# Kernel tuning notes

Hardware: AMD Instinct MI355X
Metric: run time of the kernel (lower is better)

## Reference

```python
import jax, jax.numpy as jnp
import numpy as np

# pywt db4 decomposition filters
DEC_LO = jnp.array([-0.010597401784997278, 0.032883011666982945, 0.030841381835986965, -0.18703481171888114, -0.02798376941698385, 0.6308807679295904, 0.7148465705525415, 0.23037781330885523], dtype=jnp.float32)
DEC_HI = jnp.array([-0.23037781330885523, 0.7148465705525415, -0.6308807679295904, -0.02798376941698385, 0.18703481171888114, 0.030841381835986965, -0.032883011666982945, -0.010597401784997278], dtype=jnp.float32)

def _dwt_step(x):
    # single-level DWT along last axis, pywt 'symmetric' mode; x: [N, n]
    L = DEC_LO.shape[0]
    xe = jnp.pad(x, ((0, 0), (L - 1, L - 1)), mode='symmetric')[:, 1:]
    k = jnp.stack([DEC_LO[::-1], DEC_HI[::-1]])[:, None, :]  # [2,1,L]
    y = jax.lax.conv_general_dilated(xe[:, None, :], k, window_strides=(2,), padding='VALID')
    return y[:, 0, :], y[:, 1, :]  # cA, cD, each [N, (n+L-1)//2]

def _wavedec(x, level):
    a, dets = x, []
    for _ in range(level):
        a, d = _dwt_step(a)
        dets.append(d)
    return [a] + dets[::-1]  # [cA_L, cD_L, ..., cD_1]

def _wavelet_kan(x, basis, scales=5):
    # torch code detaches x before pywt.wavedec -> stop_gradient for faithful bwd
    coeffs = _wavedec(jax.lax.stop_gradient(x), scales - 1)
    out = 0.0
    for s in range(scales):
        c = coeffs[s]
        out = out + c @ basis[s][:c.shape[1], :]
    return out

def _dendritic(x, W, b):
    # W: [branches, in, out]; max over branches of GELU(Linear)
    h = jnp.einsum('ni,kio->kno', x, W) + b[:, None, :]
    return jnp.max(jax.nn.gelu(h, approximate=False), axis=0)

def _layernorm(x, g, b, eps=1e-5):
    m = jnp.mean(x, -1, keepdims=True)
    v = jnp.var(x, -1, keepdims=True)
    return (x - m) * jax.lax.rsqrt(v + eps) * g + b

def setup_inputs():
    key = jax.random.key(0)
    ks = jax.random.split(key, 12)
    N, D, H, M, Z, K, E = 16384, 768, 512, 256, 256, 20, 262144
    inp = {}
    inp['x'] = jax.random.normal(ks[0], (N, D), jnp.float32)
    inp['adj_rows'] = jax.random.randint(ks[1], (E,), 0, N, jnp.int32)
    inp['adj_cols'] = jax.random.randint(ks[2], (E,), 0, N, jnp.int32)
    inp['adj_vals'] = jax.random.uniform(ks[3], (E,), jnp.float32)
    inp['basis_enc'] = jax.random.normal(ks[4], (5, D, H), jnp.float32)
    inp['ln_g'] = jnp.ones((H,), jnp.float32)
    inp['ln_b'] = jnp.zeros((H,), jnp.float32)
    inp['Wd_enc'] = jax.random.normal(ks[5], (K, H, M), jnp.float32) * 0.04
    inp['bd_enc'] = jnp.zeros((K, M), jnp.float32)
    inp['W_mu'] = jax.random.normal(ks[6], (M, Z), jnp.float32) * 0.06
    inp['b_mu'] = jnp.zeros((Z,), jnp.float32)
    inp['W_lv'] = jax.random.normal(ks[7], (M, Z), jnp.float32) * 0.06
    inp['b_lv'] = jnp.zeros((Z,), jnp.float32)
    inp['Wd_dec'] = jax.random.normal(ks[8], (K, Z, H), jnp.float32) * 0.06
    inp['bd_dec'] = jnp.zeros((K, H), jnp.float32)
    inp['basis_dec'] = jax.random.normal(ks[9], (5, H, D), jnp.float32)
    inp['eps'] = jax.random.normal(ks[10], (N, Z), jnp.float32)
    return inp

def reference(x, adj_rows, adj_cols, adj_vals, basis_enc, ln_g, ln_b, Wd_enc, bd_enc, W_mu, b_mu, W_lv, b_lv, Wd_dec, bd_dec, basis_dec, eps):
    N = x.shape[0]
    # torch.sparse.mm(adj, x) with COO adj
    xa = jax.ops.segment_sum(adj_vals[:, None] * x[adj_cols], adj_rows, num_segments=N)
    h = _wavelet_kan(xa, basis_enc)
    h = _layernorm(h, ln_g, ln_b)
    enc = _dendritic(h, Wd_enc, bd_enc)
    mu = enc @ W_mu + b_mu
    logvar = enc @ W_lv + b_lv
    z = mu + eps * jnp.exp(0.5 * logvar)
    dec = _dendritic(z, Wd_dec, bd_dec)
    recon = _wavelet_kan(dec, basis_dec)
    return recon, mu, logvar
```

## Files before the change

kernel.cpp:

```cpp
#include <hip/hip_runtime.h>

typedef __attribute__((ext_vector_type(8))) short short8v;
typedef __attribute__((ext_vector_type(8))) unsigned short ushort8v;
typedef __attribute__((ext_vector_type(4))) float float4v;

__device__ __constant__ float c_LO[8] = {
    -0.010597401784997278f, 0.032883011666982945f, 0.030841381835986965f,
    -0.18703481171888114f, -0.02798376941698385f, 0.6308807679295904f,
    0.7148465705525415f, 0.23037781330885523f};
__device__ __constant__ float c_HI[8] = {
    -0.23037781330885523f, 0.7148465705525415f, -0.6308807679295904f,
    -0.02798376941698385f, 0.18703481171888114f, 0.030841381835986965f,
    -0.032883011666982945f, -0.010597401784997278f};

__device__ __forceinline__ unsigned short f2bf(float f) {
    unsigned u = __builtin_bit_cast(unsigned, f);
    unsigned r = u + 0x7fffu + ((u >> 16) & 1u);
    return (unsigned short)(r >> 16);
}
__device__ __forceinline__ float bf2f(unsigned short u) {
    return __builtin_bit_cast(float, (unsigned)u << 16);
}

__device__ __forceinline__ float gelu_fast(float x) {
    float x3 = x * x * x;
    float y = fmaf(0.044715f, x3, x) * 0.7978845608028654f;
    float t = fminf(fmaxf(y * 2.8853900817779268f, -30.f), 30.f);
    float e = exp2f(t);
    return x * e * __builtin_amdgcn_rcpf(e + 1.0f);
}

__device__ __forceinline__ void gload_lds16(const void* g, void* l) {
    __builtin_amdgcn_global_load_lds(g, l, 16, 0, 0);
}

__device__ __forceinline__ void dwt_lvl(const float* __restrict__ in, int n, float* __restrict__ outA,
                                        unsigned short* __restrict__ outD, int m, int lane) {
    for (int j = lane; j < m; j += 64) {
        float a = 0.f, d = 0.f;
#pragma unroll
        for (int i = 0; i < 8; ++i) {
            int p = 2 * j + 7 - i;
            int q = (p < 6) ? (5 - p) : ((p < n + 6) ? (p - 6) : (2 * n + 5 - p));
            float xv = in[q];
            a = fmaf(c_LO[i], xv, a);
            d = fmaf(c_HI[i], xv, d);
        }
        outA[j] = a;
        outD[j] = f2bf(d);
    }
}
__device__ __forceinline__ void dwt_lvl_final(const float* __restrict__ in, int n, unsigned short* __restrict__ outA,
                                              unsigned short* __restrict__ outD, int m, int lane) {
    for (int j = lane; j < m; j += 64) {
        float a = 0.f, d = 0.f;
#pragma unroll
        for (int i = 0; i < 8; ++i) {
            int p = 2 * j + 7 - i;
            int q = (p < 6) ? (5 - p) : ((p < n + 6) ? (p - 6) : (2 * n + 5 - p));
            float xv = in[q];
            a = fmaf(c_LO[i], xv, a);
            d = fmaf(c_HI[i], xv, d);
        }
        outA[j] = f2bf(a);
        outD[j] = f2bf(d);
    }
}

__global__ void cast_bf16_kernel(const float* __restrict__ in, unsigned short* __restrict__ out, int n4) {
    int i = blockIdx.x * blockDim.x + threadIdx.x;
    if (i >= n4) return;
    float4 v = ((const float4*)in)[i];
    ushort4 o;
    o.x = f2bf(v.x); o.y = f2bf(v.y); o.z = f2bf(v.z); o.w = f2bf(v.w);
    ((ushort4*)out)[i] = o;
}

__global__ void hist_kernel(const int* __restrict__ rows, int* __restrict__ cnt, int E) {
    int i = blockIdx.x * blockDim.x + threadIdx.x;
    if (i < E) atomicAdd(&cnt[rows[i]], 1);
}

__global__ __launch_bounds__(1024) void scan_kernel(const int* __restrict__ cnt, int* __restrict__ offs,
                                                    int* __restrict__ cursor, int Nrows, int E) {
    __shared__ int part[1024];
    int tid = threadIdx.x;
    const int per = Nrows / 1024;
    int base = tid * per;
    int local[16];
    int s = 0;
    for (int i = 0; i < per; ++i) { local[i] = s; s += cnt[base + i]; }
    part[tid] = s;
    __syncthreads();
    for (int off = 1; off < 1024; off <<= 1) {
        int v = part[tid];
        int w = (tid >= off) ? part[tid - off] : 0;
        __syncthreads();
        part[tid] = v + w;
        __syncthreads();
    }
    int pre = (tid == 0) ? 0 : part[tid - 1];
    for (int i = 0; i < per; ++i) {
        int o = pre + local[i];
        offs[base + i] = o;
        cursor[base + i] = o;
    }
    if (tid == 0) offs[Nrows] = E;
}

__global__ void scatter_kernel(const int* __restrict__ rows, const int* __restrict__ cols,
                               const float* __restrict__ vals, int* __restrict__ cursor,
                               int* __restrict__ ccol, float* __restrict__ cval, int E) {
    int i = blockIdx.x * blockDim.x + threadIdx.x;
    if (i >= E) return;
    int r = rows[i];
    int p = atomicAdd(&cursor[r], 1);
    ccol[p] = cols[i];
    cval[p] = vals[i];
}

__global__ __launch_bounds__(256) void spmm_wavedec_enc(const unsigned short* __restrict__ xb,
                                                        const int* __restrict__ offs,
                                                        const int* __restrict__ ccol,
                                                        const float* __restrict__ cval,
                                                        unsigned short* __restrict__ cenc) {
    __shared__ float buf0[4][768];
    __shared__ float buf1[4][400];
    const int widx = threadIdx.x >> 6, lane = threadIdx.x & 63;
    const int r = blockIdx.x * 4 + widx;
    float* b0 = buf0[widx];
    float* b1 = buf1[widx];

    int s = offs[r], e = offs[r + 1];
    float acc[12] = {};
    for (int j = s; j < e; ++j) {
        int c = ccol[j];
        float v = cval[j];
        const unsigned short* xr = xb + (size_t)c * 768;
#pragma unroll
        for (int seg = 0; seg < 3; ++seg) {
            ushort4 u = *(const ushort4*)(xr + seg * 256 + lane * 4);
            acc[seg * 4 + 0] = fmaf(v, bf2f(u.x), acc[seg * 4 + 0]);
            acc[seg * 4 + 1] = fmaf(v, bf2f(u.y), acc[seg * 4 + 1]);
            acc[seg * 4 + 2] = fmaf(v, bf2f(u.z), acc[seg * 4 + 2]);
            acc[seg * 4 + 3] = fmaf(v, bf2f(u.w), acc[seg * 4 + 3]);
        }
    }
#pragma unroll
    for (int seg = 0; seg < 3; ++seg) {
        b0[seg * 256 + lane * 4 + 0] = acc[seg * 4 + 0];
        b0[seg * 256 + lane * 4 + 1] = acc[seg * 4 + 1];
        b0[seg * 256 + lane * 4 + 2] = acc[seg * 4 + 2];
        b0[seg * 256 + lane * 4 + 3] = acc[seg * 4 + 3];
    }
    __syncthreads();

    unsigned short* cr = cenc + (size_t)r * 800;
    dwt_lvl(b0, 768, b1, cr + 407, 387, lane);
    __syncthreads();
    dwt_lvl(b1, 387, b0, cr + 210, 197, lane);
    __syncthreads();
    dwt_lvl(b0, 197, b1, cr + 108, 102, lane);
    __syncthreads();
    dwt_lvl_final(b1, 102, cr + 0, cr + 54, 54, lane);
    if (lane < 6) cr[794 + lane] = 0;
}

__global__ __launch_bounds__(256) void wavedec_dec(const unsigned short* __restrict__ decb,
                                                   unsigned short* __restrict__ cdec) {
    __shared__ float buf0[4][512];
    __shared__ float buf1[4][272];
    const int widx = threadIdx.x >> 6, lane = threadIdx.x & 63;
    const int r = blockIdx.x * 4 + widx;
    float* b0 = buf0[widx];
    float* b1 = buf1[widx];
    const unsigned short* ip = decb + (size_t)r * 512;
    for (int i = lane; i < 512; i += 64) b0[i] = bf2f(ip[i]);
    __syncthreads();
    unsigned short* cr = cdec + (size_t)r * 544;
    dwt_lvl(b0, 512, b1, cr + 279, 259, lane);
    __syncthreads();
    dwt_lvl(b1, 259, b0, cr + 146, 133, lane);
    __syncthreads();
    dwt_lvl(b0, 133, b1, cr + 76, 70, lane);
    __syncthreads();
    dwt_lvl_final(b1, 70, cr + 0, cr + 38, 38, lane);
    if (lane < 6) cr[538 + lane] = 0;
}

struct Bounds { int b[6]; };

__global__ void pack_basis_T(const float* __restrict__ basis, unsigned short* __restrict__ BT,
                             Bounds bd, int brows, int N, int K, int Kpad) {
    int idx = blockIdx.x * blockDim.x + threadIdx.x;
    if (idx >= N * Kpad) return;
    int n = idx / Kpad, k = idx - n * Kpad;
    float v = 0.f;
    if (k < K) {
        int s = 0;
#pragma unroll
        for (int t = 1; t < 5; ++t)
            if (k >= bd.b[t]) s = t;
        int lr = k - bd.b[s];
        v = basis[((size_t)s * brows + lr) * N + n];
    }
    BT[idx] = f2bf(v);
}

__global__ void pack_wT(const float* __restrict__ W, unsigned short* __restrict__ WT,
                        int NB, int K, int N, int Kpad) {
    int idx = blockIdx.x * blockDim.x + threadIdx.x;
    int tot = NB * N * Kpad;
    if (idx >= tot) return;
    int b = idx / (N * Kpad);
    int r = idx - b * (N * Kpad);
    int n = r / Kpad, k = r - n * Kpad;
    float v = (k < K) ? W[((size_t)b * K + k) * N + n] : 0.f;
    WT[idx] = f2bf(v);
}

template <int MODE>
__global__ __launch_bounds__(256) void gemm_mfma(const unsigned short* __restrict__ A,
                                                 const unsigned short* __restrict__ BT,
                                                 const float* __restrict__ bias,
                                                 const float* __restrict__ bias2,
                                                 void* __restrict__ Cv, void* __restrict__ Cv2,
                                                 int M, int N, int K, int lda, int ldb, int ldc, int nx) {
    __shared__ __align__(16) unsigned short As[128 * 32];
    __shared__ __align__(16) unsigned short Bs[128 * 32];
    const int tid = threadIdx.x;
    const int wave = tid >> 6, lane = tid & 63;
    const int nwg = gridDim.x;
    const int logical = (blockIdx.x & 7) * (nwg >> 3) + (blockIdx.x >> 3);
    const int mblk = logical / nx, nblk = logical - mblk * nx;
    const int m0 = mblk * 128, n0 = nblk * 128;
    const int wr = wave >> 1, wc = wave & 1;
    const int frow = lane & 15, fq = lane >> 4;

    const int off0 = tid * 16;
    const int r0 = off0 >> 6, c0 = off0 & 63;
    const int r1 = (off0 + 4096) >> 6, c1 = (off0 + 4096) & 63;
    const char* Ab = (const char*)A;
    const char* Bb = (const char*)BT;
    size_t gA0 = (size_t)(m0 + r0) * lda * 2 + c0;
    size_t gA1 = (size_t)(m0 + r1) * lda * 2 + c1;
    size_t gB0 = (size_t)(n0 + r0) * ldb * 2 + c0;
    size_t gB1 = (size_t)(n0 + r1) * ldb * 2 + c1;
    char* lA0 = (char*)As + wave * 1024;
    char* lB0 = (char*)Bs + wave * 1024;

    const int aoff = (wr * 64 + frow) * 32 + fq * 8;
    const int boff = (wc * 64 + frow) * 32 + fq * 8;

    float4v acc[4][4] = {};
    for (int k0 = 0; k0 < K; k0 += 32) {
        size_t kb2 = (size_t)k0 * 2;
        gload_lds16(Ab + gA0 + kb2, lA0);
        gload_lds16(Ab + gA1 + kb2, lA0 + 4096);
        gload_lds16(Bb + gB0 + kb2, lB0);
        gload_lds16(Bb + gB1 + kb2, lB0 + 4096);
        __syncthreads();
        short8v av[4], bv[4];
#pragma unroll
        for (int i = 0; i < 4; ++i) av[i] = *(const short8v*)(As + aoff + i * 512);
#pragma unroll
        for (int i = 0; i < 4; ++i) bv[i] = *(const short8v*)(Bs + boff + i * 512);
#pragma unroll
        for (int mi = 0; mi < 4; ++mi)
#pragma unroll
            for (int ni = 0; ni < 4; ++ni)
                acc[mi][ni] = __builtin_amdgcn_mfma_f32_16x16x32_bf16(av[mi], bv[ni], acc[mi][ni], 0, 0, 0);
        __syncthreads();
    }
#pragma unroll
    for (int ni = 0; ni < 4; ++ni) {
        int col = n0 + wc * 64 + ni * 16 + frow;
        float bval;
        float* dst;
        int coll;
        if (MODE == 2) {
            bool isMu = col < 256;
            coll = col & 255;
            bval = isMu ? bias[coll] : bias2[coll];
            dst = (float*)(isMu ? Cv : Cv2);
        } else {
            coll = col;
            bval = bias ? bias[col] : 0.f;
            dst = (float*)Cv;
        }
#pragma unroll
        for (int mi = 0; mi < 4; ++mi) {
#pragma unroll
            for (int i = 0; i < 4; ++i) {
                int row = m0 + wr * 64 + mi * 16 + fq * 4 + i;
                float v = acc[mi][ni][i] + bval;
                if (MODE == 2)
                    dst[(size_t)row * 256 + coll] = v;
                else
                    dst[(size_t)row * ldc + coll] = v;
            }
        }
    }
}

__global__ __launch_bounds__(256, 2) void dendritic_full(const unsigned short* __restrict__ A,
                                                         const unsigned short* __restrict__ WT,
                                                         const float* __restrict__ bias,
                                                         unsigned short* __restrict__ out,
                                                         int M, int Nc, int K, int nb, int nx) {
    __shared__ __align__(16) unsigned short As[128 * 64];
    __shared__ __align__(16) unsigned short Bs[2][64 * 64];
    const int tid = threadIdx.x;
    const int wave = tid >> 6;
    const int lane = tid & 63;

    const int nwg = gridDim.x;
    const int logical = (blockIdx.x & 7) * (nwg >> 3) + (blockIdx.x >> 3);
    const int mblk = logical / nx;
    const int nblk = logical - mblk * nx;
    const int n0 = nblk * 64, m0 = mblk * 128;

    const int wr = wave >> 1, wc = wave & 1;
    const int frow = lane & 15, fq = lane >> 4;

    int srA[4], scA[4];
#pragma unroll
    for (int i = 0; i < 4; ++i) {
        int ch = i * 256 + tid;
        srA[i] = ch >> 3;
        scA[i] = ((ch & 7) ^ (srA[i] & 7)) * 16;
    }
    int srB[2], scB[2];
#pragma unroll
    for (int i = 0; i < 2; ++i) {
        int ch = i * 256 + tid;
        srB[i] = ch >> 3;
        scB[i] = ((ch & 7) ^ (srB[i] & 7)) * 16;
    }
    const char* Ab = (const char*)A;
    const size_t K2 = (size_t)K * 2;
    const size_t branchBytes = (size_t)Nc * K2;
    char* lA  = (char*)As + wave * 1024;
    char* lB0 = (char*)&Bs[0][0] + wave * 1024;
    char* lB1 = (char*)&Bs[1][0] + wave * 1024;

    float4v hmn[4][2], hmx[4][2];
#pragma unroll
    for (int mi = 0; mi < 4; ++mi)
#pragma unroll
        for (int ni = 0; ni < 2; ++ni) { hmn[mi][ni] = (float4v)(1e30f); hmx[mi][ni] = (float4v)(-1e30f); }

    const int npair = nb >> 1;
    for (int p = 0; p < npair; ++p) {
        const int b0 = 2 * p, b1 = 2 * p + 1;
        const char* Bb0 = (const char*)WT + (size_t)b0 * branchBytes;
        const char* Bb1 = (const char*)WT + (size_t)b1 * branchBytes;
        float4v ac0[4][2], ac1[4][2];
#pragma unroll
        for (int ni = 0; ni < 2; ++ni) {
            int col = n0 + wc * 32 + ni * 16 + frow;
            float bv0 = bias[(size_t)b0 * Nc + col];
            float bv1 = bias[(size_t)b1 * Nc + col];
#pragma unroll
            for (int mi = 0; mi < 4; ++mi) { ac0[mi][ni] = (float4v)(bv0); ac1[mi][ni] = (float4v)(bv1); }
        }
        for (int k0 = 0; k0 < K; k0 += 64) {
            const size_t kby = (size_t)k0 * 2;
#pragma unroll
            for (int i = 0; i < 4; ++i)
                gload_lds16(Ab + (size_t)(m0 + srA[i]) * K2 + kby + scA[i], lA + i * 4096);
#pragma unroll
            for (int i = 0; i < 2; ++i)
                gload_lds16(Bb0 + (size_t)(n0 + srB[i]) * K2 + kby + scB[i], lB0 + i * 4096);
#pragma unroll
            for (int i = 0; i < 2; ++i)
                gload_lds16(Bb1 + (size_t)(n0 + srB[i]) * K2 + kby + scB[i], lB1 + i * 4096);
            __syncthreads();
#pragma unroll
            for (int kk = 0; kk < 2; ++kk) {
                short8v av[4], bv0[2], bv1[2];
                const int slot = kk * 4 + fq;
#pragma unroll
                for (int mi = 0; mi < 4; ++mi) {
                    int ra = wr * 64 + mi * 16 + frow;
                    av[mi] = *(const short8v*)((const char*)As + ra * 128 + ((slot ^ (ra & 7)) * 16));
                }
#pragma unroll
                for (int ni = 0; ni < 2; ++ni) {
                    int rb = wc * 32 + ni * 16 + frow;
                    int rboff = rb * 128 + ((slot ^ (rb & 7)) * 16);
                    bv0[ni] = *(const short8v*)((const char*)&Bs[0][0] + rboff);
                    bv1[ni] = *(const short8v*)((const char*)&Bs[1][0] + rboff);
                }
#pragma unroll
                for (int mi = 0; mi < 4; ++mi)
#pragma unroll
                    for (int ni = 0; ni < 2; ++ni) {
                        ac0[mi][ni] = __builtin_amdgcn_mfma_f32_16x16x32_bf16(av[mi], bv0[ni], ac0[mi][ni], 0, 0, 0);
                        ac1[mi][ni] = __builtin_amdgcn_mfma_f32_16x16x32_bf16(av[mi], bv1[ni], ac1[mi][ni], 0, 0, 0);
                    }
            }
            __syncthreads();
        }
#pragma unroll
        for (int ni = 0; ni < 2; ++ni)
#pragma unroll
            for (int mi = 0; mi < 4; ++mi)
#pragma unroll
                for (int i = 0; i < 4; ++i) {
                    float mn = fminf(ac0[mi][ni][i], ac1[mi][ni][i]);
                    float mx = fmaxf(ac0[mi][ni][i], ac1[mi][ni][i]);
                    hmn[mi][ni][i] = fminf(hmn[mi][ni][i], mn);
                    hmx[mi][ni][i] = fmaxf(hmx[mi][ni][i], mx);
                }
    }

#pragma unroll
    for (int ni = 0; ni < 2; ++ni) {
        int col = n0 + wc * 32 + ni * 16 + frow;
#pragma unroll
        for (int mi = 0; mi < 4; ++mi) {
#pragma unroll
            for (int i = 0; i < 4; ++i) {
                int row = m0 + wr * 64 + mi * 16 + fq * 4 + i;
                float g = fmaxf(gelu_fast(hmn[mi][ni][i]), gelu_fast(hmx[mi][ni][i]));
                out[(size_t)row * Nc + col] = f2bf(g);
            }
        }
    }
}

__global__ __launch_bounds__(256) void layernorm_bf16(const float* __restrict__ h,
                                                      unsigned short* __restrict__ o,
                                                      const float* __restrict__ g,
                                                      const float* __restrict__ b) {
    int row = blockIdx.x;
    const float* p = h + (size_t)row * 512;
    int tid = threadIdx.x;
    float v0 = p[tid], v1 = p[tid + 256];
    float s = v0 + v1, sq = v0 * v0 + v1 * v1;
#pragma unroll
    for (int off = 32; off >= 1; off >>= 1) {
        s += __shfl_xor(s, off);
        sq += __shfl_xor(sq, off);
    }
    __shared__ float ls[4], lq[4];
    int wid = tid >> 6, lane = tid & 63;
    if (lane == 0) { ls[wid] = s; lq[wid] = sq; }
    __syncthreads();
    float ts = ls[0] + ls[1] + ls[2] + ls[3];
    float tq = lq[0] + lq[1] + lq[2] + lq[3];
    float mean = ts / 512.f;
    float var = tq / 512.f - mean * mean;
    float inv = rsqrtf(var + 1e-5f);
    unsigned short* op = o + (size_t)row * 512;
    op[tid] = f2bf((v0 - mean) * inv * g[tid] + b[tid]);
    op[tid + 256] = f2bf((v1 - mean) * inv * g[tid + 256] + b[tid + 256]);
}

__global__ void z_kernel(const float* __restrict__ mu, const float* __restrict__ lv,
                         const float* __restrict__ eps, unsigned short* __restrict__ z, int n4) {
    int i = blockIdx.x * blockDim.x + threadIdx.x;
    if (i >= n4) return;
    float4 m = ((const float4*)mu)[i];
    float4 l = ((const float4*)lv)[i];
    float4 e = ((const float4*)eps)[i];
    ushort4 o;
    o.x = f2bf(m.x + e.x * expf(0.5f * l.x));
    o.y = f2bf(m.y + e.y * expf(0.5f * l.y));
    o.z = f2bf(m.z + e.z * expf(0.5f * l.z));
    o.w = f2bf(m.w + e.w * expf(0.5f * l.w));
    ((ushort4*)z)[i] = o;
}

extern "C" void kernel_launch(void* const* d_in, const int* in_sizes, int n_in,
                              void* d_out, int out_size, void* d_ws, size_t ws_size,
                              hipStream_t stream) {
    const float* x        = (const float*)d_in[0];
    const int*   arows    = (const int*)d_in[1];
    const int*   acols    = (const int*)d_in[2];
    const float* avals    = (const float*)d_in[3];
    const float* basisenc = (const float*)d_in[4];
    const float* ln_g     = (const float*)d_in[5];
    const float* ln_b     = (const float*)d_in[6];
    const float* Wd_enc   = (const float*)d_in[7];
    const float* bd_enc   = (const float*)d_in[8];
    const float* W_mu     = (const float*)d_in[9];
    const float* b_mu     = (const float*)d_in[10];
    const float* W_lv     = (const float*)d_in[11];
    const float* b_lv     = (const float*)d_in[12];
    const float* Wd_dec   = (const float*)d_in[13];
    const float* bd_dec   = (const float*)d_in[14];
    const float* basisdec = (const float*)d_in[15];
    const float* epsin    = (const float*)d_in[16];

    const int N = 16384;
    const int E = in_sizes[1];

    float* ws = (float*)d_ws;
    const size_t A0 = 0;
    const size_t B0 = A0 + (size_t)N * 768;
    const size_t C0 = B0 + (size_t)N * 400;
    const size_t F0 = C0 + (size_t)N * 387;
    const size_t G0 = F0 + 3100672;

    float* hF  = ws + A0;
    unsigned short* cenc = (unsigned short*)(ws + B0);
    unsigned short* cdec = (unsigned short*)(ws + B0);
    unsigned short* zb   = cdec + (size_t)N * 544;
    unsigned short* xbf  = (unsigned short*)(ws + C0);
    unsigned short* hbf  = (unsigned short*)(ws + C0);
    unsigned short* encb = hbf + (size_t)N * 512;
    unsigned short* decb = (unsigned short*)(ws + C0);
    unsigned short* wF = (unsigned short*)(ws + F0);
    unsigned short* BceT   = wF;
    unsigned short* BcdT   = BceT + 512 * 800;
    unsigned short* WdencT = BcdT + 768 * 544;
    unsigned short* WddecT = WdencT + 20 * 256 * 512;
    unsigned short* WmuT   = WddecT + 20 * 512 * 256;
    unsigned short* WlvT   = WmuT + 256 * 256;
    int*   csr_cnt  = (int*)(ws + G0);
    int*   csr_offs = csr_cnt + N;
    int*   csr_cur  = csr_offs + N + 1;
    int*   csr_col  = csr_cur + N;
    float* csr_val  = (float*)(csr_col + E);

    float* out_recon = (float*)d_out;
    float* out_mu    = out_recon + (size_t)N * 768;
    float* out_lv    = out_mu + (size_t)N * 256;

    {
        Bounds be = {{0, 54, 108, 210, 407, 794}};
        pack_basis_T<<<(512 * 800 + 255) / 256, 256, 0, stream>>>(basisenc, BceT, be, 768, 512, 794, 800);
        Bounds bdd = {{0, 38, 76, 146, 279, 538}};
        pack_basis_T<<<(768 * 544 + 255) / 256, 256, 0, stream>>>(basisdec, BcdT, bdd, 512, 768, 538, 544);
        pack_wT<<<(20 * 256 * 512 + 255) / 256, 256, 0, stream>>>(Wd_enc, WdencT, 20, 512, 256, 512);
        pack_wT<<<(20 * 512 * 256 + 255) / 256, 256, 0, stream>>>(Wd_dec, WddecT, 20, 256, 512, 256);
        pack_wT<<<(256 * 256 + 255) / 256, 256, 0, stream>>>(W_mu, WmuT, 1, 256, 256, 256);
        pack_wT<<<(256 * 256 + 255) / 256, 256, 0, stream>>>(W_lv, WlvT, 1, 256, 256, 256);
        cast_bf16_kernel<<<(N * 768 / 4 + 255) / 256, 256, 0, stream>>>(x, xbf, N * 768 / 4);
    }

    hipMemsetAsync(csr_cnt, 0, N * sizeof(int), stream);
    hist_kernel<<<(E + 255) / 256, 256, 0, stream>>>(arows, csr_cnt, E);
    scan_kernel<<<1, 1024, 0, stream>>>(csr_cnt, csr_offs, csr_cur, N, E);
    scatter_kernel<<<(E + 255) / 256, 256, 0, stream>>>(arows, acols, avals, csr_cur, csr_col, csr_val, E);
    spmm_wavedec_enc<<<N / 4, 256, 0, stream>>>(xbf, csr_offs, csr_col, csr_val, cenc);

    gemm_mfma<0><<<(512 / 128) * (N / 128), 256, 0, stream>>>(cenc, BceT, nullptr, nullptr, hF, nullptr,
                                                              N, 512, 800, 800, 800, 512, 512 / 128);

    layernorm_bf16<<<N, 256, 0, stream>>>(hF, hbf, ln_g, ln_b);

    dendritic_full<<<4 * (N / 128), 256, 0, stream>>>(hbf, WdencT, bd_enc, encb, N, 256, 512, 20, 4);

    gemm_mfma<2><<<(512 / 128) * (N / 128), 256, 0, stream>>>(encb, WmuT, b_mu, b_lv, out_mu, out_lv,
                                                              N, 512, 256, 256, 256, 256, 512 / 128);

    z_kernel<<<(N * 256 / 4 + 255) / 256, 256, 0, stream>>>(out_mu, out_lv, epsin, zb, N * 256 / 4);

    dendritic_full<<<8 * (N / 128), 256, 0, stream>>>(zb, WddecT, bd_dec, decb, N, 512, 256, 20, 8);

    wavedec_dec<<<N / 4, 256, 0, stream>>>(decb, cdec);

    gemm_mfma<0><<<(768 / 128) * (N / 128), 256, 0, stream>>>(cdec, BcdT, nullptr, nullptr, out_recon, nullptr,
                                                              N, 768, 544, 544, 544, 768, 768 / 128);

    (void)ws_size; (void)out_size; (void)n_in;
}
```

Measured before the change: 475.8 us.

## Fuse mu/logvar GEMM with reparameterization, tile weight packing, add resident-A decoder dendritic

Weight and basis transposes now go through shared-memory 64x64 tiles, so both the reads and the writes are coalesced instead of strided. The mu and logvar projections are computed together in one kernel that also adds the biases and computes z, which removes the separate z kernel and its re-read of mu and logvar. A new decoder dendritic kernel keeps the whole K=256 A tile resident in LDS and processes two branches per pass. The cost is more LDS and register pressure per block, which may lower occupancy.

```diff
diff --git a/kernel.cpp b/kernel.cpp
--- a/kernel.cpp
+++ b/kernel.cpp
@@ -190,41 +190,65 @@
 
 struct Bounds { int b[6]; };
 
-__global__ void pack_basis_T(const float* __restrict__ basis, unsigned short* __restrict__ BT,
-                             Bounds bd, int brows, int N, int K, int Kpad) {
-    int idx = blockIdx.x * blockDim.x + threadIdx.x;
-    if (idx >= N * Kpad) return;
-    int n = idx / Kpad, k = idx - n * Kpad;
-    float v = 0.f;
-    if (k < K) {
-        int s = 0;
-#pragma unroll
-        for (int t = 1; t < 5; ++t)
-            if (k >= bd.b[t]) s = t;
-        int lr = k - bd.b[s];
-        v = basis[((size_t)s * brows + lr) * N + n];
-    }
-    BT[idx] = f2bf(v);
-}
-
-__global__ void pack_wT(const float* __restrict__ W, unsigned short* __restrict__ WT,
-                        int NB, int K, int N, int Kpad) {
-    int idx = blockIdx.x * blockDim.x + threadIdx.x;
-    int tot = NB * N * Kpad;
-    if (idx >= tot) return;
-    int b = idx / (N * Kpad);
-    int r = idx - b * (N * Kpad);
-    int n = r / Kpad, k = r - n * Kpad;
-    float v = (k < K) ? W[((size_t)b * K + k) * N + n] : 0.f;
-    WT[idx] = f2bf(v);
-}
-
-template <int MODE>
+__global__ __launch_bounds__(256) void pack_wT_t(const float* __restrict__ W, unsigned short* __restrict__ WT,
+                                                 int K, int N, int Kpad) {
+    __shared__ float t[64][65];
+    const int b = blockIdx.z;
+    const int k0 = blockIdx.x * 64, n0 = blockIdx.y * 64;
+    const int tid = threadIdx.x;
+#pragma unroll
+    for (int i = 0; i < 16; ++i) {
+        int idx = tid + i * 256;
+        int kk = idx >> 6, nn = idx & 63;
+        int k = k0 + kk;
+        t[kk][nn] = (k < K) ? W[((size_t)b * K + k) * N + n0 + nn] : 0.f;
+    }
+    __syncthreads();
+#pragma unroll
+    for (int i = 0; i < 16; ++i) {
+        int idx = tid + i * 256;
+        int nn = idx >> 6, kk = idx & 63;
+        int k = k0 + kk;
+        if (k < Kpad)
+            WT[((size_t)b * N + n0 + nn) * Kpad + k] = f2bf(t[kk][nn]);
+    }
+}
+
+__global__ __launch_bounds__(256) void pack_basis_t(const float* __restrict__ basis, unsigned short* __restrict__ BT,
+                                                    Bounds bd, int brows, int N, int K, int Kpad) {
+    __shared__ float t[64][65];
+    const int k0 = blockIdx.x * 64, n0 = blockIdx.y * 64;
+    const int tid = threadIdx.x;
+#pragma unroll
+    for (int i = 0; i < 16; ++i) {
+        int idx = tid + i * 256;
+        int kk = idx >> 6, nn = idx & 63;
+        int k = k0 + kk;
+        float v = 0.f;
+        if (k < K) {
+            int s = 0;
+#pragma unroll
+            for (int u = 1; u < 5; ++u)
+                if (k >= bd.b[u]) s = u;
+            int lr = k - bd.b[s];
+            v = basis[((size_t)s * brows + lr) * N + n0 + nn];
+        }
+        t[kk][nn] = v;
+    }
+    __syncthreads();
+#pragma unroll
+    for (int i = 0; i < 16; ++i) {
+        int idx = tid + i * 256;
+        int nn = idx >> 6, kk = idx & 63;
+        int k = k0 + kk;
+        if (k < Kpad)
+            BT[(size_t)(n0 + nn) * Kpad + k] = f2bf(t[kk][nn]);
+    }
+}
+
 __global__ __launch_bounds__(256) void gemm_mfma(const unsigned short* __restrict__ A,
                                                  const unsigned short* __restrict__ BT,
-                                                 const float* __restrict__ bias,
-                                                 const float* __restrict__ bias2,
-                                                 void* __restrict__ Cv, void* __restrict__ Cv2,
+                                                 float* __restrict__ C,
                                                  int M, int N, int K, int lda, int ldb, int ldc, int nx) {
     __shared__ __align__(16) unsigned short As[128 * 32];
     __shared__ __align__(16) unsigned short Bs[128 * 32];
@@ -275,29 +299,93 @@
 #pragma unroll
     for (int ni = 0; ni < 4; ++ni) {
         int col = n0 + wc * 64 + ni * 16 + frow;
-        float bval;
-        float* dst;
-        int coll;
-        if (MODE == 2) {
-            bool isMu = col < 256;
-            coll = col & 255;
-            bval = isMu ? bias[coll] : bias2[coll];
-            dst = (float*)(isMu ? Cv : Cv2);
-        } else {
-            coll = col;
-            bval = bias ? bias[col] : 0.f;
-            dst = (float*)Cv;
-        }
 #pragma unroll
         for (int mi = 0; mi < 4; ++mi) {
 #pragma unroll
             for (int i = 0; i < 4; ++i) {
                 int row = m0 + wr * 64 + mi * 16 + fq * 4 + i;
-                float v = acc[mi][ni][i] + bval;
-                if (MODE == 2)
-                    dst[(size_t)row * 256 + coll] = v;
-                else
-                    dst[(size_t)row * ldc + coll] = v;
+                C[(size_t)row * ldc + col] = acc[mi][ni][i];
+            }
+        }
+    }
+}
+
+__global__ __launch_bounds__(256) void gemm_muvlz(const unsigned short* __restrict__ A,
+                                                  const unsigned short* __restrict__ BmuT,
+                                                  const unsigned short* __restrict__ BlvT,
+                                                  const float* __restrict__ bmu,
+                                                  const float* __restrict__ blv,
+                                                  const float* __restrict__ eps,
+                                                  float* __restrict__ omu, float* __restrict__ olv,
+                                                  unsigned short* __restrict__ zb, int nx) {
+    __shared__ __align__(16) unsigned short As[128 * 32];
+    __shared__ __align__(16) unsigned short Bmu[128 * 32];
+    __shared__ __align__(16) unsigned short Blv[128 * 32];
+    const int tid = threadIdx.x;
+    const int wave = tid >> 6, lane = tid & 63;
+    const int nwg = gridDim.x;
+    const int logical = (blockIdx.x & 7) * (nwg >> 3) + (blockIdx.x >> 3);
+    const int mblk = logical / nx, nblk = logical - mblk * nx;
+    const int m0 = mblk * 128, n0 = nblk * 128;
+    const int wr = wave >> 1, wc = wave & 1;
+    const int frow = lane & 15, fq = lane >> 4;
+
+    const int off0 = tid * 16;
+    const int r0 = off0 >> 6, c0 = off0 & 63;
+    const int r1 = (off0 + 4096) >> 6, c1 = (off0 + 4096) & 63;
+    const char* Ab = (const char*)A;
+    size_t gA0 = (size_t)(m0 + r0) * 512 + c0;
+    size_t gA1 = (size_t)(m0 + r1) * 512 + c1;
+    size_t gB0 = (size_t)(n0 + r0) * 512 + c0;
+    size_t gB1 = (size_t)(n0 + r1) * 512 + c1;
+    char* lA0 = (char*)As + wave * 1024;
+    char* lM0 = (char*)Bmu + wave * 1024;
+    char* lV0 = (char*)Blv + wave * 1024;
+
+    const int aoff = (wr * 64 + frow) * 32 + fq * 8;
+    const int boff = (wc * 64 + frow) * 32 + fq * 8;
+
+    float4v am[4][4] = {}, al[4][4] = {};
+    for (int k0 = 0; k0 < 256; k0 += 32) {
+        size_t kb2 = (size_t)k0 * 2;
+        gload_lds16(Ab + gA0 + kb2, lA0);
+        gload_lds16(Ab + gA1 + kb2, lA0 + 4096);
+        gload_lds16((const char*)BmuT + gB0 + kb2, lM0);
+        gload_lds16((const char*)BmuT + gB1 + kb2, lM0 + 4096);
+        gload_lds16((const char*)BlvT + gB0 + kb2, lV0);
+        gload_lds16((const char*)BlvT + gB1 + kb2, lV0 + 4096);
+        __syncthreads();
+        short8v av[4], bm[4], bl[4];
+#pragma unroll
+        for (int i = 0; i < 4; ++i) av[i] = *(const short8v*)(As + aoff + i * 512);
+#pragma unroll
+        for (int i = 0; i < 4; ++i) bm[i] = *(const short8v*)(Bmu + boff + i * 512);
+#pragma unroll
+        for (int i = 0; i < 4; ++i) bl[i] = *(const short8v*)(Blv + boff + i * 512);
+#pragma unroll
+        for (int mi = 0; mi < 4; ++mi)
+#pragma unroll
+            for (int ni = 0; ni < 4; ++ni) {
+                am[mi][ni] = __builtin_amdgcn_mfma_f32_16x16x32_bf16(av[mi], bm[ni], am[mi][ni], 0, 0, 0);
+                al[mi][ni] = __builtin_amdgcn_mfma_f32_16x16x32_bf16(av[mi], bl[ni], al[mi][ni], 0, 0, 0);
+            }
+        __syncthreads();
+    }
+#pragma unroll
+    for (int ni = 0; ni < 4; ++ni) {
+        int col = n0 + wc * 64 + ni * 16 + frow;
+        float bm = bmu[col], bl = blv[col];
+#pragma unroll
+        for (int mi = 0; mi < 4; ++mi) {
+#pragma unroll
+            for (int i = 0; i < 4; ++i) {
+                int row = m0 + wr * 64 + mi * 16 + fq * 4 + i;
+                float mu = am[mi][ni][i] + bm;
+                float lv = al[mi][ni][i] + bl;
+                float e = eps[(size_t)row * 256 + col];
+                omu[(size_t)row * 256 + col] = mu;
+                olv[(size_t)row * 256 + col] = lv;
+                zb[(size_t)row * 256 + col] = f2bf(mu + e * expf(0.5f * lv));
             }
         }
     }
@@ -430,6 +518,134 @@
     }
 }
 
+__global__ __launch_bounds__(256, 2) void dendritic_dec_res(const unsigned short* __restrict__ A,
+                                                            const unsigned short* __restrict__ WT,
+                                                            const float* __restrict__ bias,
+                                                            unsigned short* __restrict__ out,
+                                                            int M, int Nc, int nb, int nx) {
+    constexpr int K = 256;
+    __shared__ __align__(16) unsigned short As[128 * 256];
+    __shared__ __align__(16) unsigned short Bs[2][64 * 64];
+    const int tid = threadIdx.x;
+    const int wave = tid >> 6;
+    const int lane = tid & 63;
+
+    const int nwg = gridDim.x;
+    const int logical = (blockIdx.x & 7) * (nwg >> 3) + (blockIdx.x >> 3);
+    const int mblk = logical / nx;
+    const int nblk = logical - mblk * nx;
+    const int n0 = nblk * 64, m0 = mblk * 128;
+
+    const int wr = wave >> 1, wc = wave & 1;
+    const int frow = lane & 15, fq = lane >> 4;
+
+    const char* Ab = (const char*)A;
+    const size_t K2 = (size_t)K * 2;
+    for (int i = 0; i < 16; ++i) {
+        int ch = i * 256 + tid;
+        int row = ch >> 5, slot = ch & 31;
+        int sslot = (slot & ~7) | ((slot & 7) ^ (row & 7));
+        gload_lds16(Ab + (size_t)(m0 + row) * K2 + sslot * 16, (char*)As + i * 4096 + wave * 1024);
+    }
+
+    int srB[2], scB[2];
+#pragma unroll
+    for (int i = 0; i < 2; ++i) {
+        int ch = i * 256 + tid;
+        srB[i] = ch >> 3;
+        scB[i] = ((ch & 7) ^ (srB[i] & 7)) * 16;
+    }
+    const size_t branchBytes = (size_t)Nc * K2;
+    char* lB0 = (char*)&Bs[0][0] + wave * 1024;
+    char* lB1 = (char*)&Bs[1][0] + wave * 1024;
+
+    float4v hmn[4][2], hmx[4][2];
+#pragma unroll
+    for (int mi = 0; mi < 4; ++mi)
+#pragma unroll
+        for (int ni = 0; ni < 2; ++ni) { hmn[mi][ni] = (float4v)(1e30f); hmx[mi][ni] = (float4v)(-1e30f); }
+
+    const int npair = nb >> 1;
+    for (int p = 0; p < npair; ++p) {
+        const int b0 = 2 * p, b1 = 2 * p + 1;
+        const char* Bb0 = (const char*)WT + (size_t)b0 * branchBytes;
+        const char* Bb1 = (const char*)WT + (size_t)b1 * branchBytes;
+        float4v ac0[4][2], ac1[4][2];
+#pragma unroll
+        for (int ni = 0; ni < 2; ++ni) {
+            int col = n0 + wc * 32 + ni * 16 + frow;
+            float bv0 = bias[(size_t)b0 * Nc + col];
+            float bv1 = bias[(size_t)b1 * Nc + col];
+#pragma unroll
+            for (int mi = 0; mi < 4; ++mi) { ac0[mi][ni] = (float4v)(bv0); ac1[mi][ni] = (float4v)(bv1); }
+        }
+        for (int k0 = 0; k0 < K; k0 += 64) {
+            const size_t kby = (size_t)k0 * 2;
+#pragma unroll
+            for (int i = 0; i < 2; ++i)
+                gload_lds16(Bb0 + (size_t)(n0 + srB[i]) * K2 + kby + scB[i], lB0 + i * 4096);
+#pragma unroll
+            for (int i = 0; i < 2; ++i)
+                gload_lds16(Bb1 + (size_t)(n0 + srB[i]) * K2 + kby + scB[i], lB1 + i * 4096);
+            __syncthreads();
+#pragma unroll
+            for (int kk = 0; kk < 2; ++kk) {
+                short8v av[4], bv0[2], bv1[2];
+                const int slot = kk * 4 + fq;
+                const int gbase = k0 >> 4;
+#pragma unroll
+                for (int mi = 0; mi < 4; ++mi) {
+                    int ra = wr * 64 + mi * 16 + frow;
+                    int g = (k0 >> 3) + slot;
+                    int sl = (g & ~7) | ((g & 7) ^ (ra & 7));
+                    av[mi] = *(const short8v*)((const char*)As + ra * 512 + sl * 16);
+                }
+                (void)gbase;
+#pragma unroll
+                for (int ni = 0; ni < 2; ++ni) {
+                    int rb = wc * 32 + ni * 16 + frow;
+                    int rboff = rb * 128 + ((slot ^ (rb & 7)) * 16);
+                    bv0[ni] = *(const short8v*)((const char*)&Bs[0][0] + rboff);
+                    bv1[ni] = *(const short8v*)((const char*)&Bs[1][0] + rboff);
+                }
+#pragma unroll
+                for (int mi = 0; mi < 4; ++mi)
+#pragma unroll
+                    for (int ni = 0; ni < 2; ++ni) {
+                        ac0[mi][ni] = __builtin_amdgcn_mfma_f32_16x16x32_bf16(av[mi], bv0[ni], ac0[mi][ni], 0, 0, 0);
+                        ac1[mi][ni] = __builtin_amdgcn_mfma_f32_16x16x32_bf16(av[mi], bv1[ni], ac1[mi][ni], 0, 0, 0);
+                    }
+            }
+            __syncthreads();
+        }
+#pragma unroll
+        for (int ni = 0; ni < 2; ++ni)
+#pragma unroll
+            for (int mi = 0; mi < 4; ++mi)
+#pragma unroll
+                for (int i = 0; i < 4; ++i) {
+                    float mn = fminf(ac0[mi][ni][i], ac1[mi][ni][i]);
+                    float mx = fmaxf(ac0[mi][ni][i], ac1[mi][ni][i]);
+                    hmn[mi][ni][i] = fminf(hmn[mi][ni][i], mn);
+                    hmx[mi][ni][i] = fmaxf(hmx[mi][ni][i], mx);
+                }
+    }
+
+#pragma unroll
+    for (int ni = 0; ni < 2; ++ni) {
+        int col = n0 + wc * 32 + ni * 16 + frow;
+#pragma unroll
+        for (int mi = 0; mi < 4; ++mi) {
+#pragma unroll
+            for (int i = 0; i < 4; ++i) {
+                int row = m0 + wr * 64 + mi * 16 + fq * 4 + i;
+                float g = fmaxf(gelu_fast(hmn[mi][ni][i]), gelu_fast(hmx[mi][ni][i]));
+                out[(size_t)row * Nc + col] = f2bf(g);
+            }
+        }
+    }
+}
+
 __global__ __launch_bounds__(256) void layernorm_bf16(const float* __restrict__ h,
                                                       unsigned short* __restrict__ o,
                                                       const float* __restrict__ g,
@@ -456,21 +672,6 @@
     unsigned short* op = o + (size_t)row * 512;
     op[tid] = f2bf((v0 - mean) * inv * g[tid] + b[tid]);
     op[tid + 256] = f2bf((v1 - mean) * inv * g[tid + 256] + b[tid + 256]);
-}
-
-__global__ void z_kernel(const float* __restrict__ mu, const float* __restrict__ lv,
-                         const float* __restrict__ eps, unsigned short* __restrict__ z, int n4) {
-    int i = blockIdx.x * blockDim.x + threadIdx.x;
-    if (i >= n4) return;
-    float4 m = ((const float4*)mu)[i];
-    float4 l = ((const float4*)lv)[i];
-    float4 e = ((const float4*)eps)[i];
-    ushort4 o;
-    o.x = f2bf(m.x + e.x * expf(0.5f * l.x));
-    o.y = f2bf(m.y + e.y * expf(0.5f * l.y));
-    o.z = f2bf(m.z + e.z * expf(0.5f * l.z));
-    o.w = f2bf(m.w + e.w * expf(0.5f * l.w));
-    ((ushort4*)z)[i] = o;
 }
 
 extern "C" void kernel_launch(void* const* d_in, const int* in_sizes, int n_in,
@@ -531,13 +732,13 @@
 
     {
         Bounds be = {{0, 54, 108, 210, 407, 794}};
-        pack_basis_T<<<(512 * 800 + 255) / 256, 256, 0, stream>>>(basisenc, BceT, be, 768, 512, 794, 800);
+        pack_basis_t<<<dim3(13, 8), 256, 0, stream>>>(basisenc, BceT, be, 768, 512, 794, 800);
         Bounds bdd = {{0, 38, 76, 146, 279, 538}};
-        pack_basis_T<<<(768 * 544 + 255) / 256, 256, 0, stream>>>(basisdec, BcdT, bdd, 512, 768, 538, 544);
-        pack_wT<<<(20 * 256 * 512 + 255) / 256, 256, 0, stream>>>(Wd_enc, WdencT, 20, 512, 256, 512);
-        pack_wT<<<(20 * 512 * 256 + 255) / 256, 256, 0, stream>>>(Wd_dec, WddecT, 20, 256, 512, 256);
-        pack_wT<<<(256 * 256 + 255) / 256, 256, 0, stream>>>(W_mu, WmuT, 1, 256, 256, 256);
-        pack_wT<<<(256 * 256 + 255) / 256, 256, 0, stream>>>(W_lv, WlvT, 1, 256, 256, 256);
+        pack_basis_t<<<dim3(9, 12), 256, 0, stream>>>(basisdec, BcdT, bdd, 512, 768, 538, 544);
+        pack_wT_t<<<dim3(8, 4, 20), 256, 0, stream>>>(Wd_enc, WdencT, 512, 256, 512);
+        pack_wT_t<<<dim3(4, 8, 20), 256, 0, stream>>>(Wd_dec, WddecT, 256, 512, 256);
+        pack_wT_t<<<dim3(4, 4, 1), 256, 0, stream>>>(W_mu, WmuT, 256, 256, 256);
+        pack_wT_t<<<dim3(4, 4, 1), 256, 0, stream>>>(W_lv, WlvT, 256, 256, 256);
         cast_bf16_kernel<<<(N * 768 / 4 + 255) / 256, 256, 0, stream>>>(x, xbf, N * 768 / 4);
     }
 
@@ -547,24 +748,19 @@
     scatter_kernel<<<(E + 255) / 256, 256, 0, stream>>>(arows, acols, avals, csr_cur, csr_col, csr_val, E);
     spmm_wavedec_enc<<<N / 4, 256, 0, stream>>>(xbf, csr_offs, csr_col, csr_val, cenc);
 
-    gemm_mfma<0><<<(512 / 128) * (N / 128), 256, 0, stream>>>(cenc, BceT, nullptr, nullptr, hF, nullptr,
-                                                              N, 512, 800, 800, 800, 512, 512 / 128);
+    gemm_mfma<<<(512 / 128) * (N / 128), 256, 0, stream>>>(cenc, BceT, hF, N, 512, 800, 800, 800, 512, 512 / 128);
 
     layernorm_bf16<<<N, 256, 0, stream>>>(hF, hbf, ln_g, ln_b);
 
     dendritic_full<<<4 * (N / 128), 256, 0, stream>>>(hbf, WdencT, bd_enc, encb, N, 256, 512, 20, 4);
 
-    gemm_mfma<2><<<(512 / 128) * (N / 128), 256, 0, stream>>>(encb, WmuT, b_mu, b_lv, out_mu, out_lv,
-                                                              N, 512, 256, 256, 256, 256, 512 / 128);
-
-    z_kernel<<<(N * 256 / 4 + 255) / 256, 256, 0, stream>>>(out_mu, out_lv, epsin, zb, N * 256 / 4);
-
-    dendritic_full<<<8 * (N / 128), 256, 0, stream>>>(zb, WddecT, bd_dec, decb, N, 512, 256, 20, 8);
+    gemm_muvlz<<<2 * (N / 128), 256, 0, stream>>>(encb, WmuT, WlvT, b_mu, b_lv, epsin, out_mu, out_lv, zb, 2);
+
+    dendritic_dec_res<<<8 * (N / 128), 256, 0, stream>>>(zb, WddecT, bd_dec, decb, N, 512, 20, 8);
 
     wavedec_dec<<<N / 4, 256, 0, stream>>>(decb, cdec);
 
-    gemm_mfma<0><<<(768 / 128) * (N / 128), 256, 0, stream>>>(cdec, BcdT, nullptr, nullptr, out_recon, nullptr,
-                                                              N, 768, 544, 544, 544, 768, 768 / 128);
+    gemm_mfma<<<(768 / 128) * (N / 128), 256, 0, stream>>>(cdec, BcdT, out_recon, N, 768, 544, 544, 544, 768, 768 / 128);
 
     (void)ws_size; (void)out_size; (void)n_in;
 }
```

New measurement: 489.3 us. 2.9% more time.
